# Optimization experiments

Measured on AMD Instinct MI355X. Metric: run time of the kernel, lower is better.

## Reference

```python
import jax, jax.numpy as jnp
import numpy as np

B, T, IN = 32, 1024, 256
H = 128          # hidden_size
NL = 2           # num_layers
NC = 4           # num_classes
F2 = 2 * H       # bidirectional feature size


def _lstm_dir(xs, w_ih, w_hh, b_ih, b_hh, reverse):
    # xs: [T, B, in]; w_ih: [4H, in]; w_hh: [4H, H]
    if reverse:
        xs = xs[::-1]
    h0 = jnp.zeros((xs.shape[1], H), xs.dtype)
    c0 = jnp.zeros((xs.shape[1], H), xs.dtype)

    def step(carry, xt):
        h, c = carry
        g = xt @ w_ih.T + b_ih + h @ w_hh.T + b_hh  # [B, 4H]
        i, f, gg, o = jnp.split(g, 4, axis=-1)       # PyTorch gate order i,f,g,o
        c = jax.nn.sigmoid(f) * c + jax.nn.sigmoid(i) * jnp.tanh(gg)
        h = jax.nn.sigmoid(o) * jnp.tanh(c)
        return (h, c), h

    _, hs = jax.lax.scan(step, (h0, c0), xs)  # [T, B, H]
    if reverse:
        hs = hs[::-1]
    return hs


def setup_inputs() -> dict:
    key = jax.random.key(0)
    ks = jax.random.split(key, 12)
    s = 0.05
    x = jax.random.normal(ks[0], (B, T, IN), jnp.float32)
    # stacked LSTM params: [layer, direction, ...]; layer0 in = IN, layer1 in = 2H = IN
    w_ih = jax.random.normal(ks[1], (NL, 2, 4 * H, IN), jnp.float32) * s
    w_hh = jax.random.normal(ks[2], (NL, 2, 4 * H, H), jnp.float32) * s
    b_ih = jax.random.normal(ks[3], (NL, 2, 4 * H), jnp.float32) * s
    b_hh = jax.random.normal(ks[4], (NL, 2, 4 * H), jnp.float32) * s
    wq = jax.random.normal(ks[5], (F2, F2), jnp.float32) * s
    wk = jax.random.normal(ks[6], (F2, F2), jnp.float32) * s
    wv = jax.random.normal(ks[7], (F2, F2), jnp.float32) * s
    bq = jax.random.normal(ks[8], (F2,), jnp.float32) * s
    bk = jax.random.normal(ks[9], (F2,), jnp.float32) * s
    bv = jax.random.normal(ks[10], (F2,), jnp.float32) * s
    w_fc = jax.random.normal(ks[11], (NC, F2), jnp.float32) * s
    b_fc = jnp.zeros((NC,), jnp.float32)
    return {"x": x, "w_ih": w_ih, "w_hh": w_hh, "b_ih": b_ih, "b_hh": b_hh,
            "wq": wq, "wk": wk, "wv": wv, "bq": bq, "bk": bk, "bv": bv,
            "w_fc": w_fc, "b_fc": b_fc}


def reference(x, w_ih, w_hh, b_ih, b_hh, wq, wk, wv, bq, bk, bv, w_fc, b_fc):
    # --- biLSTM (eval mode: inter-layer dropout inactive) ---
    xs = jnp.swapaxes(x, 0, 1)  # time-major [T, B, IN]
    for l in range(NL):
        fwd = _lstm_dir(xs, w_ih[l, 0], w_hh[l, 0], b_ih[l, 0], b_hh[l, 0], False)
        bwd = _lstm_dir(xs, w_ih[l, 1], w_hh[l, 1], b_ih[l, 1], b_hh[l, 1], True)
        xs = jnp.concatenate([fwd, bwd], axis=-1)  # [T, B, 2H]
    out = jnp.swapaxes(xs, 0, 1)  # [B, T, 2H]
    # --- naive full self-attention ---
    q = out @ wq.T + bq
    k = out @ wk.T + bk
    v = out @ wv.T + bv
    scores = jnp.einsum('btd,bsd->bts', q, k) / jnp.sqrt(jnp.float32(F2))
    attn = jax.nn.softmax(scores, axis=-1)          # [B, T, T]
    ctx = jnp.einsum('bts,bsd->btd', attn, v)       # [B, T, 2H]
    # --- FC head on last timestep ---
    return ctx[:, -1, :] @ w_fc.T + b_fc            # [B, NC]
```

## Files before the change

kernel.cpp:

```cpp
#include <hip/hip_runtime.h>
#include <math.h>
#include <stdint.h>

#define BB 32
#define TT 1024
#define INF 256
#define HH 128
#define G4 512
#define CH 16

typedef _Float16 half2_t __attribute__((ext_vector_type(2)));
typedef __attribute__((address_space(3))) uint32_t lds_u32;
typedef __attribute__((address_space(1))) const uint32_t glb_u32;

__device__ __forceinline__ float fdot2f(half2_t a, half2_t b, float c) {
    return __builtin_amdgcn_fdot2(a, b, c, false);
}
__device__ __forceinline__ float rcpf(float x) {
    return __builtin_amdgcn_rcpf(x);
}
__device__ __forceinline__ float dpp_xor1(float x) {
    return __builtin_bit_cast(float, __builtin_amdgcn_update_dpp(
        0, __builtin_bit_cast(int, x), 0xB1, 0xF, 0xF, true));
}
__device__ __forceinline__ float dpp_xor2(float x) {
    return __builtin_bit_cast(float, __builtin_amdgcn_update_dpp(
        0, __builtin_bit_cast(int, x), 0x4E, 0xF, 0xF, true));
}
__device__ __forceinline__ void bar_lgkm() {
    asm volatile("s_waitcnt lgkmcnt(0)\n\ts_barrier" ::: "memory");
}

__global__ __launch_bounds__(256) void gemm_inproj(
    const float* __restrict__ A,
    const float* __restrict__ w_ih_l,
    const float* __restrict__ b_ih_l,
    const float* __restrict__ b_hh_l,
    float* __restrict__ xproj)
{
    const int d  = blockIdx.z;
    const float* W = w_ih_l + (size_t)d * G4 * INF;
    float* C = xproj + (size_t)d * 32768 * 512;
    const int m0 = blockIdx.y * 128;
    const int n0 = blockIdx.x * 128;
    const int tid = threadIdx.x;
    const int tx = tid & 15, ty = tid >> 4;

    __shared__ __align__(16) float As[16 * 132];
    __shared__ __align__(16) float Bs[16 * 132];

    float acc[8][8] = {};
    const int lr = tid >> 1;
    const int lk = (tid & 1) * 8;

    float4 a0 = *(const float4*)(A + (size_t)(m0 + lr) * 256 + lk);
    float4 a1 = *(const float4*)(A + (size_t)(m0 + lr) * 256 + lk + 4);
    float4 b0 = *(const float4*)(W + (size_t)(n0 + lr) * 256 + lk);
    float4 b1 = *(const float4*)(W + (size_t)(n0 + lr) * 256 + lk + 4);

    for (int k0 = 0; k0 < 256; k0 += 16) {
        __syncthreads();
        As[(lk + 0) * 132 + lr] = a0.x; As[(lk + 1) * 132 + lr] = a0.y;
        As[(lk + 2) * 132 + lr] = a0.z; As[(lk + 3) * 132 + lr] = a0.w;
        As[(lk + 4) * 132 + lr] = a1.x; As[(lk + 5) * 132 + lr] = a1.y;
        As[(lk + 6) * 132 + lr] = a1.z; As[(lk + 7) * 132 + lr] = a1.w;
        Bs[(lk + 0) * 132 + lr] = b0.x; Bs[(lk + 1) * 132 + lr] = b0.y;
        Bs[(lk + 2) * 132 + lr] = b0.z; Bs[(lk + 3) * 132 + lr] = b0.w;
        Bs[(lk + 4) * 132 + lr] = b1.x; Bs[(lk + 5) * 132 + lr] = b1.y;
        Bs[(lk + 6) * 132 + lr] = b1.z; Bs[(lk + 7) * 132 + lr] = b1.w;
        __syncthreads();
        if (k0 + 16 < 256) {
            a0 = *(const float4*)(A + (size_t)(m0 + lr) * 256 + k0 + 16 + lk);
            a1 = *(const float4*)(A + (size_t)(m0 + lr) * 256 + k0 + 16 + lk + 4);
            b0 = *(const float4*)(W + (size_t)(n0 + lr) * 256 + k0 + 16 + lk);
            b1 = *(const float4*)(W + (size_t)(n0 + lr) * 256 + k0 + 16 + lk + 4);
        }
#pragma unroll
        for (int kk = 0; kk < 16; ++kk) {
            float4 av0 = *(const float4*)&As[kk * 132 + ty * 4];
            float4 av1 = *(const float4*)&As[kk * 132 + 64 + ty * 4];
            float4 bv0 = *(const float4*)&Bs[kk * 132 + tx * 4];
            float4 bv1 = *(const float4*)&Bs[kk * 132 + 64 + tx * 4];
            float ar[8] = {av0.x, av0.y, av0.z, av0.w, av1.x, av1.y, av1.z, av1.w};
            float br[8] = {bv0.x, bv0.y, bv0.z, bv0.w, bv1.x, bv1.y, bv1.z, bv1.w};
#pragma unroll
            for (int i = 0; i < 8; ++i)
#pragma unroll
                for (int j = 0; j < 8; ++j)
                    acc[i][j] += ar[i] * br[j];
        }
    }

    float bias[8];
#pragma unroll
    for (int j = 0; j < 8; ++j) {
        const int n = n0 + (j < 4 ? tx * 4 + j : 64 + tx * 4 + (j - 4));
        bias[j] = b_ih_l[d * G4 + n] + b_hh_l[d * G4 + n];
    }
#pragma unroll
    for (int i = 0; i < 8; ++i) {
        const int m = m0 + (i < 4 ? ty * 4 + i : 64 + ty * 4 + (i - 4));
        float4 o0, o1;
        o0.x = acc[i][0] + bias[0]; o0.y = acc[i][1] + bias[1];
        o0.z = acc[i][2] + bias[2]; o0.w = acc[i][3] + bias[3];
        o1.x = acc[i][4] + bias[4]; o1.y = acc[i][5] + bias[5];
        o1.z = acc[i][6] + bias[6]; o1.w = acc[i][7] + bias[7];
        *(float4*)(C + (size_t)m * 512 + n0 + tx * 4)      = o0;
        *(float4*)(C + (size_t)m * 512 + n0 + 64 + tx * 4) = o1;
    }
}

__global__ __launch_bounds__(512, 2) void lstm_rec(
    const float* __restrict__ xproj,
    const float* __restrict__ w_hh_l,
    float* __restrict__ out)
{
    const int b = blockIdx.x & 31;
    const int d = blockIdx.x >> 5;
    const int tid = threadIdx.x;
    const int wvid = tid >> 6;
    const int l = tid & 63;
    const int s = l & 3;
    const int g = l >> 2;
    const int j = (wvid << 4) | g;

    __shared__ __align__(16) _Float16 hs[HH];
    __shared__ __align__(16) float xbuf[2][CH * 512];
    __shared__ __align__(16) float obuf[CH * HH];

    half2_t wv[4][16];
#pragma unroll
    for (int G = 0; G < 4; ++G) {
        const float* wr = w_hh_l + (size_t)(d * G4 + 128 * G + j) * HH + 32 * s;
#pragma unroll
        for (int q4 = 0; q4 < 8; ++q4) {
            float4 f = *(const float4*)(wr + 4 * q4);
            wv[G][2 * q4]     = half2_t{(_Float16)f.x, (_Float16)f.y};
            wv[G][2 * q4 + 1] = half2_t{(_Float16)f.z, (_Float16)f.w};
        }
    }

    if (tid < 64) ((half2_t*)hs)[tid] = half2_t{(_Float16)0.f, (_Float16)0.f};
    float c = 0.f;

    const float* xp = xproj + ((size_t)d * BB + b) * TT * 512;
    float* ob = out + (size_t)b * TT * 256 + d * HH;

    {
        const int tlo = d ? 1008 : 0;
        const float* gsrc = xp + (size_t)tlo * 512;
#pragma unroll
        for (int i = 0; i < 4; ++i)
            __builtin_amdgcn_global_load_lds((glb_u32*)(gsrc + tid * 4 + i * 2048),
                                             (lds_u32*)&xbuf[0][tid * 4 + i * 2048],
                                             16, 0, 0);
    }
    __syncthreads();

    for (int ck = 0; ck < 64; ++ck) {
        const int cur = ck & 1;
        if (ck + 1 < 64) {
            const int tlo = d ? (1008 - (ck + 1) * CH) : (ck + 1) * CH;
            const float* gsrc = xp + (size_t)tlo * 512;
#pragma unroll
            for (int i = 0; i < 4; ++i)
                __builtin_amdgcn_global_load_lds((glb_u32*)(gsrc + tid * 4 + i * 2048),
                                                 (lds_u32*)&xbuf[cur ^ 1][tid * 4 + i * 2048],
                                                 16, 0, 0);
        }
        const float* xb = xbuf[cur];

#pragma unroll 1
        for (int si = 0; si < CH; ++si) {
            const int lds_t = d ? (CH - 1 - si) : si;

            const float4* hp = (const float4*)(hs + 32 * s);
            float4 hA = hp[0], hB = hp[1], hC = hp[2], hD = hp[3];
            half2_t hh[16];
            hh[0]  = __builtin_bit_cast(half2_t, hA.x);
            hh[1]  = __builtin_bit_cast(half2_t, hA.y);
            hh[2]  = __builtin_bit_cast(half2_t, hA.z);
            hh[3]  = __builtin_bit_cast(half2_t, hA.w);
            hh[4]  = __builtin_bit_cast(half2_t, hB.x);
            hh[5]  = __builtin_bit_cast(half2_t, hB.y);
            hh[6]  = __builtin_bit_cast(half2_t, hB.z);
            hh[7]  = __builtin_bit_cast(half2_t, hB.w);
            hh[8]  = __builtin_bit_cast(half2_t, hC.x);
            hh[9]  = __builtin_bit_cast(half2_t, hC.y);
            hh[10] = __builtin_bit_cast(half2_t, hC.z);
            hh[11] = __builtin_bit_cast(half2_t, hC.w);
            hh[12] = __builtin_bit_cast(half2_t, hD.x);
            hh[13] = __builtin_bit_cast(half2_t, hD.y);
            hh[14] = __builtin_bit_cast(half2_t, hD.z);
            hh[15] = __builtin_bit_cast(half2_t, hD.w);

            float a0 = 0.f, a1 = 0.f, a2 = 0.f, a3 = 0.f;
#pragma unroll
            for (int kk = 0; kk < 16; ++kk) {
                a0 = fdot2f(wv[0][kk], hh[kk], a0);
                a1 = fdot2f(wv[1][kk], hh[kk], a1);
                a2 = fdot2f(wv[2][kk], hh[kk], a2);
                a3 = fdot2f(wv[3][kk], hh[kk], a3);
            }

            a0 += dpp_xor1(a0); a0 += dpp_xor2(a0);
            a1 += dpp_xor1(a1); a1 += dpp_xor2(a1);
            a2 += dpp_xor1(a2); a2 += dpp_xor2(a2);
            a3 += dpp_xor1(a3); a3 += dpp_xor2(a3);

            const float xv = xb[lds_t * 512 + 128 * s + j];
            const float pre = (s == 0 ? a0 : s == 1 ? a1 : s == 2 ? a2 : a3) + xv;

            const bool isG = (s == 2);
            const float e = __expf(isG ? 2.f * pre : -pre);
            const float r = rcpf(1.f + e);
            const float v = isG ? 1.f - 2.f * r : r;

            const float t = dpp_xor2(v);
            const float u = dpp_xor1(v * t);

            if (s == 1) {
                c = v * c + u;
                const float th = 1.f - 2.f * rcpf(1.f + __expf(2.f * c));
                const float h = t * th;
                hs[j] = (_Float16)h;
                obuf[si * HH + j] = h;
            }
            bar_lgkm();
        }

        {
            const int idx = tid * 4;
            const int sf = idx >> 7, jf = idx & 127;
            const int sg = ck * CH + sf;
            const int t  = d ? (TT - 1 - sg) : sg;
            float4 o0 = *(const float4*)&obuf[idx];
            *(float4*)&ob[(size_t)t * 256 + jf] = o0;
        }
        __syncthreads();
    }
}

__global__ __launch_bounds__(256) void attn_kernel(
    const float* __restrict__ out1,
    const float* __restrict__ wq, const float* __restrict__ bq,
    const float* __restrict__ wk,
    const float* __restrict__ wv, const float* __restrict__ bv,
    const float* __restrict__ wfc, const float* __restrict__ bfc,
    float* __restrict__ outp)
{
    const int b = blockIdx.x;
    const int tid = threadIdx.x;
    __shared__ float xl[256], q[256], u[256], cx[256];
    __shared__ __align__(16) float r[256];
    __shared__ float sc[TT];
    __shared__ float red[256];

    const float* ob = out1 + (size_t)b * TT * 256;

    xl[tid] = ob[(size_t)(TT - 1) * 256 + tid];
    __syncthreads();

    float acc = bq[tid];
    const float* wqr = wq + (size_t)tid * 256;
#pragma unroll 4
    for (int k = 0; k < 256; ++k) acc += xl[k] * wqr[k];
    q[tid] = acc;
    __syncthreads();

    acc = 0.f;
#pragma unroll 4
    for (int dd = 0; dd < 256; ++dd) acc += q[dd] * wk[(size_t)dd * 256 + tid];
    r[tid] = acc;
    __syncthreads();

    const int wave = tid >> 6, lane = tid & 63;
    float4 r4 = *(const float4*)&r[lane * 4];
    for (int t = wave; t < TT; t += 4) {
        float4 o4 = *(const float4*)(ob + (size_t)t * 256 + lane * 4);
        float p = r4.x * o4.x + r4.y * o4.y + r4.z * o4.z + r4.w * o4.w;
#pragma unroll
        for (int off = 32; off > 0; off >>= 1) p += __shfl_down(p, off, 64);
        if (lane == 0) sc[t] = p * 0.0625f;
    }
    __syncthreads();

    float mx = -1e30f;
#pragma unroll
    for (int i = 0; i < 4; ++i) mx = fmaxf(mx, sc[tid + 256 * i]);
    red[tid] = mx; __syncthreads();
    for (int st = 128; st > 0; st >>= 1) {
        if (tid < st) red[tid] = fmaxf(red[tid], red[tid + st]);
        __syncthreads();
    }
    mx = red[0]; __syncthreads();
    float lsum = 0.f;
#pragma unroll
    for (int i = 0; i < 4; ++i) {
        float e = expf(sc[tid + 256 * i] - mx);
        sc[tid + 256 * i] = e;
        lsum += e;
    }
    __syncthreads();
    red[tid] = lsum; __syncthreads();
    for (int st = 128; st > 0; st >>= 1) {
        if (tid < st) red[tid] += red[tid + st];
        __syncthreads();
    }
    const float inv = 1.f / red[0];
    __syncthreads();

    acc = 0.f;
#pragma unroll 8
    for (int t = 0; t < TT; ++t) acc += sc[t] * ob[(size_t)t * 256 + tid];
    u[tid] = acc * inv;
    __syncthreads();

    acc = bv[tid];
#pragma unroll 4
    for (int k = 0; k < 256; ++k) acc += u[k] * wv[(size_t)tid * 256 + k];
    cx[tid] = acc;
    __syncthreads();

    if (tid < 4) {
        float o = bfc[tid];
        for (int k = 0; k < 256; ++k) o += cx[k] * wfc[tid * 256 + k];
        outp[b * 4 + tid] = o;
    }
}

extern "C" void kernel_launch(void* const* d_in, const int* in_sizes, int n_in,
                              void* d_out, int out_size, void* d_ws, size_t ws_size,
                              hipStream_t stream)
{
    const float* x    = (const float*)d_in[0];
    const float* w_ih = (const float*)d_in[1];
    const float* w_hh = (const float*)d_in[2];
    const float* b_ih = (const float*)d_in[3];
    const float* b_hh = (const float*)d_in[4];
    const float* wq   = (const float*)d_in[5];
    const float* wk   = (const float*)d_in[6];
    const float* wv   = (const float*)d_in[7];
    const float* bq   = (const float*)d_in[8];
    const float* bv   = (const float*)d_in[10];
    const float* wfc  = (const float*)d_in[11];
    const float* bfcv = (const float*)d_in[12];
    float* outp = (float*)d_out;

    float* ws    = (float*)d_ws;
    float* xproj = ws;
    float* out0  = ws + 33554432;
    float* out1  = out0 + 8388608;

    dim3 gg(4, 256, 2);

    gemm_inproj<<<gg, 256, 0, stream>>>(x, w_ih, b_ih, b_hh, xproj);
    lstm_rec<<<64, 512, 0, stream>>>(xproj, w_hh, out0);
    gemm_inproj<<<gg, 256, 0, stream>>>(out0, w_ih + 2 * 512 * 256, b_ih + 1024, b_hh + 1024, xproj);
    lstm_rec<<<64, 512, 0, stream>>>(xproj, w_hh + 2 * 512 * 128, out1);
    attn_kernel<<<32, 256, 0, stream>>>(out1, wq, bq, wk, wv, bv, wfc, bfcv, outp);
}
```

Measured before the change: 1.901 ms.

## Use fp16 dot2 in input-projection GEMM and restructure LSTM gate computation

The input-projection GEMM now converts A and W tiles to fp16 pairs in LDS and accumulates with fdot2, halving LDS footprint and inner-loop FMA count while doubling the K-tile to 32. The LSTM recurrence splits the dot-product accumulation into two independent chains for more ILP. Every lane now computes all four gates redundantly, which removes the DPP gate exchange and the divergent branch. The recurrence launch bound drops to one block per SIMD to allow more registers. fp16 rounding of the input activations adds precision risk, and the redundant transcendental work adds ALU cost on the latency-critical serial path.

Measured after the change: 1.783 ms. -6.2%, faster.

```diff
diff --git a/kernel.cpp b/kernel.cpp
--- a/kernel.cpp
+++ b/kernel.cpp
@@ -31,7 +31,7 @@
     asm volatile("s_waitcnt lgkmcnt(0)\n\ts_barrier" ::: "memory");
 }
 
-__global__ __launch_bounds__(256) void gemm_inproj(
+__global__ __launch_bounds__(256, 2) void gemm_inproj(
     const float* __restrict__ A,
     const float* __restrict__ w_ih_l,
     const float* __restrict__ b_ih_l,
@@ -46,48 +46,50 @@
     const int tid = threadIdx.x;
     const int tx = tid & 15, ty = tid >> 4;
 
-    __shared__ __align__(16) float As[16 * 132];
-    __shared__ __align__(16) float Bs[16 * 132];
+    __shared__ __align__(16) half2_t As2[16 * 128];
+    __shared__ __align__(16) half2_t Bs2[16 * 128];
 
     float acc[8][8] = {};
     const int lr = tid >> 1;
-    const int lk = (tid & 1) * 8;
-
-    float4 a0 = *(const float4*)(A + (size_t)(m0 + lr) * 256 + lk);
-    float4 a1 = *(const float4*)(A + (size_t)(m0 + lr) * 256 + lk + 4);
-    float4 b0 = *(const float4*)(W + (size_t)(n0 + lr) * 256 + lk);
-    float4 b1 = *(const float4*)(W + (size_t)(n0 + lr) * 256 + lk + 4);
-
-    for (int k0 = 0; k0 < 256; k0 += 16) {
-        __syncthreads();
-        As[(lk + 0) * 132 + lr] = a0.x; As[(lk + 1) * 132 + lr] = a0.y;
-        As[(lk + 2) * 132 + lr] = a0.z; As[(lk + 3) * 132 + lr] = a0.w;
-        As[(lk + 4) * 132 + lr] = a1.x; As[(lk + 5) * 132 + lr] = a1.y;
-        As[(lk + 6) * 132 + lr] = a1.z; As[(lk + 7) * 132 + lr] = a1.w;
-        Bs[(lk + 0) * 132 + lr] = b0.x; Bs[(lk + 1) * 132 + lr] = b0.y;
-        Bs[(lk + 2) * 132 + lr] = b0.z; Bs[(lk + 3) * 132 + lr] = b0.w;
-        Bs[(lk + 4) * 132 + lr] = b1.x; Bs[(lk + 5) * 132 + lr] = b1.y;
-        Bs[(lk + 6) * 132 + lr] = b1.z; Bs[(lk + 7) * 132 + lr] = b1.w;
-        __syncthreads();
-        if (k0 + 16 < 256) {
-            a0 = *(const float4*)(A + (size_t)(m0 + lr) * 256 + k0 + 16 + lk);
-            a1 = *(const float4*)(A + (size_t)(m0 + lr) * 256 + k0 + 16 + lk + 4);
-            b0 = *(const float4*)(W + (size_t)(n0 + lr) * 256 + k0 + 16 + lk);
-            b1 = *(const float4*)(W + (size_t)(n0 + lr) * 256 + k0 + 16 + lk + 4);
-        }
-#pragma unroll
-        for (int kk = 0; kk < 16; ++kk) {
-            float4 av0 = *(const float4*)&As[kk * 132 + ty * 4];
-            float4 av1 = *(const float4*)&As[kk * 132 + 64 + ty * 4];
-            float4 bv0 = *(const float4*)&Bs[kk * 132 + tx * 4];
-            float4 bv1 = *(const float4*)&Bs[kk * 132 + 64 + tx * 4];
-            float ar[8] = {av0.x, av0.y, av0.z, av0.w, av1.x, av1.y, av1.z, av1.w};
-            float br[8] = {bv0.x, bv0.y, bv0.z, bv0.w, bv1.x, bv1.y, bv1.z, bv1.w};
+    const int lk = (tid & 1) * 16;
+
+    float4 ar4[4], br4[4];
+#pragma unroll
+    for (int i = 0; i < 4; ++i) {
+        ar4[i] = *(const float4*)(A + (size_t)(m0 + lr) * 256 + lk + 4 * i);
+        br4[i] = *(const float4*)(W + (size_t)(n0 + lr) * 256 + lk + 4 * i);
+    }
+
+    for (int k0 = 0; k0 < 256; k0 += 32) {
+        __syncthreads();
+#pragma unroll
+        for (int i = 0; i < 4; ++i) {
+            const int kp = (lk >> 1) + 2 * i;
+            As2[(kp + 0) * 128 + lr] = half2_t{(_Float16)ar4[i].x, (_Float16)ar4[i].y};
+            As2[(kp + 1) * 128 + lr] = half2_t{(_Float16)ar4[i].z, (_Float16)ar4[i].w};
+            Bs2[(kp + 0) * 128 + lr] = half2_t{(_Float16)br4[i].x, (_Float16)br4[i].y};
+            Bs2[(kp + 1) * 128 + lr] = half2_t{(_Float16)br4[i].z, (_Float16)br4[i].w};
+        }
+        __syncthreads();
+        if (k0 + 32 < 256) {
+#pragma unroll
+            for (int i = 0; i < 4; ++i) {
+                ar4[i] = *(const float4*)(A + (size_t)(m0 + lr) * 256 + k0 + 32 + lk + 4 * i);
+                br4[i] = *(const float4*)(W + (size_t)(n0 + lr) * 256 + k0 + 32 + lk + 4 * i);
+            }
+        }
+#pragma unroll
+        for (int kp = 0; kp < 16; ++kp) {
+            half2_t av[8], bv[8];
+            *(float4*)&av[0] = *(const float4*)&As2[kp * 128 + ty * 4];
+            *(float4*)&av[4] = *(const float4*)&As2[kp * 128 + 64 + ty * 4];
+            *(float4*)&bv[0] = *(const float4*)&Bs2[kp * 128 + tx * 4];
+            *(float4*)&bv[4] = *(const float4*)&Bs2[kp * 128 + 64 + tx * 4];
 #pragma unroll
             for (int i = 0; i < 8; ++i)
 #pragma unroll
                 for (int j = 0; j < 8; ++j)
-                    acc[i][j] += ar[i] * br[j];
+                    acc[i][j] = fdot2f(av[i], bv[j], acc[i][j]);
         }
     }
 
@@ -110,7 +112,7 @@
     }
 }
 
-__global__ __launch_bounds__(512, 2) void lstm_rec(
+__global__ __launch_bounds__(512, 1) void lstm_rec(
     const float* __restrict__ xproj,
     const float* __restrict__ w_hh_l,
     float* __restrict__ out)
@@ -173,6 +175,11 @@
 #pragma unroll 1
         for (int si = 0; si < CH; ++si) {
             const int lds_t = d ? (CH - 1 - si) : si;
+
+            const float xi = xb[lds_t * 512 +       j];
+            const float xf = xb[lds_t * 512 + 128 + j];
+            const float xg = xb[lds_t * 512 + 256 + j];
+            const float xo = xb[lds_t * 512 + 384 + j];
 
             const float4* hp = (const float4*)(hs + 32 * s);
             float4 hA = hp[0], hB = hp[1], hC = hp[2], hD = hp[3];
@@ -195,34 +202,33 @@
             hh[15] = __builtin_bit_cast(half2_t, hD.w);
 
             float a0 = 0.f, a1 = 0.f, a2 = 0.f, a3 = 0.f;
-#pragma unroll
-            for (int kk = 0; kk < 16; ++kk) {
+            float e0 = 0.f, e1 = 0.f, e2 = 0.f, e3 = 0.f;
+#pragma unroll
+            for (int kk = 0; kk < 8; ++kk) {
                 a0 = fdot2f(wv[0][kk], hh[kk], a0);
                 a1 = fdot2f(wv[1][kk], hh[kk], a1);
                 a2 = fdot2f(wv[2][kk], hh[kk], a2);
                 a3 = fdot2f(wv[3][kk], hh[kk], a3);
+                e0 = fdot2f(wv[0][kk + 8], hh[kk + 8], e0);
+                e1 = fdot2f(wv[1][kk + 8], hh[kk + 8], e1);
+                e2 = fdot2f(wv[2][kk + 8], hh[kk + 8], e2);
+                e3 = fdot2f(wv[3][kk + 8], hh[kk + 8], e3);
             }
+            a0 += e0; a1 += e1; a2 += e2; a3 += e3;
 
             a0 += dpp_xor1(a0); a0 += dpp_xor2(a0);
             a1 += dpp_xor1(a1); a1 += dpp_xor2(a1);
             a2 += dpp_xor1(a2); a2 += dpp_xor2(a2);
             a3 += dpp_xor1(a3); a3 += dpp_xor2(a3);
 
-            const float xv = xb[lds_t * 512 + 128 * s + j];
-            const float pre = (s == 0 ? a0 : s == 1 ? a1 : s == 2 ? a2 : a3) + xv;
-
-            const bool isG = (s == 2);
-            const float e = __expf(isG ? 2.f * pre : -pre);
-            const float r = rcpf(1.f + e);
-            const float v = isG ? 1.f - 2.f * r : r;
-
-            const float t = dpp_xor2(v);
-            const float u = dpp_xor1(v * t);
-
-            if (s == 1) {
-                c = v * c + u;
-                const float th = 1.f - 2.f * rcpf(1.f + __expf(2.f * c));
-                const float h = t * th;
+            const float gi = rcpf(1.f + __expf(-(a0 + xi)));
+            const float gf = rcpf(1.f + __expf(-(a1 + xf)));
+            const float gg = 1.f - 2.f * rcpf(1.f + __expf(2.f * (a2 + xg)));
+            const float go = rcpf(1.f + __expf(-(a3 + xo)));
+            c = gf * c + gi * gg;
+            const float th = 1.f - 2.f * rcpf(1.f + __expf(2.f * c));
+            const float h = go * th;
+            if (s == 0) {
                 hs[j] = (_Float16)h;
                 obuf[si * HH + j] = h;
             }
```
